# Performance work log

Measured on AMD Instinct MI355X. Metric: run time of the kernel, lower is better.

Reference implementation:

```python
import jax, jax.numpy as jnp
import numpy as np

N = 50000
E = 400000
IN_DIM = 128
HID = 128
OUT = 128
HEADS = 8
NEG_SLOPE = 0.2  # PyG GATConv default
BN_EPS = 1e-5


def _gat_conv(x, W, a_src, a_dst, b, src, dst, concat):
    """PyG GATConv (eval): self-loops added by caller. x:[N,F], W:[F,H*C], a_*:[H,C]."""
    H, C = a_src.shape
    xW = (x @ W).reshape(N, H, C)                       # [N,H,C]
    es = jnp.sum(xW * a_src[None], axis=-1)             # [N,H]
    ed = jnp.sum(xW * a_dst[None], axis=-1)             # [N,H]
    e = jax.nn.leaky_relu(es[src] + ed[dst], NEG_SLOPE) # [E,H]
    m = jax.ops.segment_max(e, dst, num_segments=N)     # softmax over incoming edges per dst
    ex = jnp.exp(e - m[dst])
    denom = jax.ops.segment_sum(ex, dst, num_segments=N)
    alpha = ex / denom[dst]                             # [E,H]
    out = jax.ops.segment_sum(xW[src] * alpha[:, :, None], dst, num_segments=N)  # [N,H,C]
    out = out.reshape(N, H * C) if concat else out.mean(axis=1)
    return out + b


def _bn_eval(h, g, be, rm, rv):
    return (h - rm) * jax.lax.rsqrt(rv + BN_EPS) * g + be


def setup_inputs() -> dict:
    key = jax.random.key(0)
    ks = jax.random.split(key, 20)
    C1 = HID // HEADS
    f32 = jnp.float32
    inp = {
        "x": jax.random.normal(ks[0], (N, IN_DIM), dtype=f32),
        "edge_index": jax.random.randint(ks[1], (2, E), 0, N, dtype=jnp.int64),
        # GAT layer 1 (in->hid, 8 heads, concat)
        "W1": jax.random.normal(ks[2], (IN_DIM, HEADS * C1), dtype=f32) * 0.05,
        "a_src1": jax.random.normal(ks[3], (HEADS, C1), dtype=f32) * 0.05,
        "a_dst1": jax.random.normal(ks[4], (HEADS, C1), dtype=f32) * 0.05,
        "b1": jnp.zeros((HEADS * C1,), dtype=f32),
        # GAT layer 2 (hid->hid, 8 heads, concat)
        "W2": jax.random.normal(ks[5], (HID, HEADS * C1), dtype=f32) * 0.05,
        "a_src2": jax.random.normal(ks[6], (HEADS, C1), dtype=f32) * 0.05,
        "a_dst2": jax.random.normal(ks[7], (HEADS, C1), dtype=f32) * 0.05,
        "b2": jnp.zeros((HEADS * C1,), dtype=f32),
        # GAT layer 3 (hid->out, 1 head, no concat)
        "W3": jax.random.normal(ks[8], (HID, OUT), dtype=f32) * 0.05,
        "a_src3": jax.random.normal(ks[9], (1, OUT), dtype=f32) * 0.05,
        "a_dst3": jax.random.normal(ks[10], (1, OUT), dtype=f32) * 0.05,
        "b3": jnp.zeros((OUT,), dtype=f32),
        # residual linears
        "R1w": jax.random.normal(ks[11], (IN_DIM, HID), dtype=f32) * 0.05,
        "R1b": jnp.zeros((HID,), dtype=f32),
        "R2w": jax.random.normal(ks[12], (HID, HID), dtype=f32) * 0.05,
        "R2b": jnp.zeros((HID,), dtype=f32),
        "R3w": jax.random.normal(ks[13], (HID, OUT), dtype=f32) * 0.05,
        "R3b": jnp.zeros((OUT,), dtype=f32),
        # batch norms (eval mode: running stats)
        "g1": jnp.ones((HID,), dtype=f32), "be1": jnp.zeros((HID,), dtype=f32),
        "rm1": jnp.zeros((HID,), dtype=f32), "rv1": jnp.ones((HID,), dtype=f32),
        "g2": jnp.ones((HID,), dtype=f32), "be2": jnp.zeros((HID,), dtype=f32),
        "rm2": jnp.zeros((HID,), dtype=f32), "rv2": jnp.ones((HID,), dtype=f32),
    }
    return inp


def reference(x, edge_index, W1, a_src1, a_dst1, b1, W2, a_src2, a_dst2, b2,
              W3, a_src3, a_dst3, b3, R1w, R1b, R2w, R2b, R3w, R3b,
              g1, be1, rm1, rv1, g2, be2, rm2, rv2):
    # PyG GATConv adds self-loops by default
    loops = jnp.arange(N, dtype=edge_index.dtype)
    src = jnp.concatenate([edge_index[0], loops])
    dst = jnp.concatenate([edge_index[1], loops])

    h = _gat_conv(x, W1, a_src1, a_dst1, b1, src, dst, concat=True) + (x @ R1w + R1b)
    h1 = jax.nn.relu(_bn_eval(h, g1, be1, rm1, rv1))  # dropout identity in eval

    h = _gat_conv(h1, W2, a_src2, a_dst2, b2, src, dst, concat=True) + (h1 @ R2w + R2b)
    h2 = jax.nn.relu(_bn_eval(h, g2, be2, rm2, rv2))

    out = _gat_conv(h2, W3, a_src3, a_dst3, b3, src, dst, concat=False) + (h2 @ R3w + R3b)
    return out
```

## Files before the change

kernel.cpp:

```cpp
#include <hip/hip_runtime.h>
#include <hip/hip_bf16.h>
#include <type_traits>

typedef __hip_bfloat16 bf16;
typedef __hip_bfloat162 bf162;
typedef short v8s __attribute__((ext_vector_type(8)));
typedef short v4s __attribute__((ext_vector_type(4)));
typedef float v4f __attribute__((ext_vector_type(4)));

#define CAP 64

__device__ __forceinline__ float lrelu(float x) { return x > 0.f ? x : 0.2f * x; }
__device__ __forceinline__ float b2f(bf16 v) { return __bfloat162float(v); }

__global__ void k_preW(const float* __restrict__ s0, const float* __restrict__ s1,
                       const float* __restrict__ s2, const float* __restrict__ s3,
                       const float* __restrict__ s4, const float* __restrict__ s5,
                       const float* __restrict__ as1, const float* __restrict__ ad1,
                       const float* __restrict__ as2, const float* __restrict__ ad2,
                       const float* __restrict__ as3, const float* __restrict__ ad3,
                       const float* b1, const float* R1b, const float* g1, const float* be1,
                       const float* rm1, const float* rv1,
                       const float* b2, const float* R2b, const float* g2, const float* be2,
                       const float* rm2, const float* rv2,
                       const float* b3, const float* R3b,
                       bf16* __restrict__ wt, float* __restrict__ prm,
                       int* __restrict__ cnt, int N) {
    int b = blockIdx.x;
    int t = threadIdx.x;
    if (b >= 7) {
        int n4 = N * 4;
        int base = ((b - 7) * 256 + t) * 4;
        int4 z = {0, 0, 0, 0};
#pragma unroll
        for (int k = 0; k < 4; ++k)
            if (base + k < n4) ((int4*)cnt)[base + k] = z;
        return;
    }
    if (b == 6) {
        int c = t;
        if (c < 128) {
            float s1v = g1[c] * rsqrtf(rv1[c] + 1e-5f);
            prm[c]       = b1[c] + R1b[c];
            prm[128 + c] = s1v;
            prm[256 + c] = be1[c] - rm1[c] * s1v;
            float s2v = g2[c] * rsqrtf(rv2[c] + 1e-5f);
            prm[384 + c] = b2[c] + R2b[c];
            prm[512 + c] = s2v;
            prm[640 + c] = be2[c] - rm2[c] * s2v;
            prm[768 + c] = b3[c] + R3b[c];
        }
        return;
    }
    const float* src;
    switch (b) {
        case 0: src = s0; break; case 1: src = s1; break; case 2: src = s2; break;
        case 3: src = s3; break; case 4: src = s4; break; default: src = s5; break;
    }
    bf16* dst = wt + (size_t)b * 18432;
    for (int i = t; i < 16384; i += 256) {
        int k = i >> 7, n = i & 127;
        dst[n * 128 + k] = __float2bfloat16(src[i]);
    }
    if ((b & 1) == 0) {
        int layer = b >> 1;
        if (layer < 2) {
            const float* asr = (layer == 0) ? as1 : as2;
            const float* ads = (layer == 0) ? ad1 : ad2;
            for (int i = t; i < 2048; i += 256) {
                int row = i >> 7, k = i & 127, h = row & 7;
                const float* av = (row < 8) ? asr : ads;
                float s = 0.f;
#pragma unroll
                for (int c = 0; c < 16; ++c) s += src[k * 128 + h * 16 + c] * av[h * 16 + c];
                dst[(128 + row) * 128 + k] = __float2bfloat16(s);
            }
        } else {
            for (int i = t; i < 2048; i += 256) {
                int row = i >> 7, k = i & 127;
                float s = 0.f;
                if (row == 0 || row == 8) {
                    const float* av = (row == 0) ? as3 : ad3;
                    for (int c = 0; c < 128; ++c) s += src[k * 128 + c] * av[c];
                }
                dst[(128 + row) * 128 + k] = __float2bfloat16(s);
            }
        }
    } else {
        for (int i = t; i < 2048; i += 256)
            dst[16384 + i] = __float2bfloat16(0.f);
    }
}

template <typename T>
__device__ __forceinline__ void gemm_body(const T* __restrict__ A,
                                          const bf16* __restrict__ BT0, const bf16* __restrict__ BT1,
                                          bf16* __restrict__ O0, bf16* __restrict__ O1,
                                          float* __restrict__ esed, float* __restrict__ es,
                                          float* __restrict__ ed,
                                          int mode, int nrows, int job, int ntiles) {
    const int y = (job >= ntiles) ? 1 : 0;
    const int tile = y ? job - ntiles : job;
    const bf16* BT = y ? BT1 : BT0;
    bf16* O = y ? O1 : O0;
    const int t = threadIdx.x;
    const int rowbase = tile * 128;
    const int wave = t >> 6, lane = t & 63, quad = lane >> 4, l16 = lane & 15;

    int gr[2], gc[2];
    gr[0] = rowbase + wave * 32 + l16; gc[0] = gr[0] < nrows ? gr[0] : nrows - 1;
    gr[1] = gr[0] + 16;                gc[1] = gr[1] < nrows ? gr[1] : nrows - 1;
    v8s afr[2][4];
    if constexpr (std::is_same<T, float>::value) {
#pragma unroll
        for (int rt = 0; rt < 2; ++rt) {
            const float* ar = A + (size_t)gc[rt] * 128 + quad * 8;
#pragma unroll
            for (int kit = 0; kit < 4; ++kit) {
                float4 u = *(const float4*)(ar + kit * 32);
                float4 w = *(const float4*)(ar + kit * 32 + 4);
                union { bf16 h[8]; v8s v; } tmp;
                tmp.h[0] = __float2bfloat16(u.x); tmp.h[1] = __float2bfloat16(u.y);
                tmp.h[2] = __float2bfloat16(u.z); tmp.h[3] = __float2bfloat16(u.w);
                tmp.h[4] = __float2bfloat16(w.x); tmp.h[5] = __float2bfloat16(w.y);
                tmp.h[6] = __float2bfloat16(w.z); tmp.h[7] = __float2bfloat16(w.w);
                afr[rt][kit] = tmp.v;
            }
        }
    } else {
#pragma unroll
        for (int rt = 0; rt < 2; ++rt) {
            const bf16* ar = A + (size_t)gc[rt] * 128 + quad * 8;
#pragma unroll
            for (int kit = 0; kit < 4; ++kit)
                afr[rt][kit] = *(const v8s*)(ar + kit * 32);
        }
    }

    v4f acc[2][9];
#pragma unroll
    for (int i = 0; i < 2; ++i)
#pragma unroll
        for (int j = 0; j < 9; ++j) acc[i][j] = (v4f){0.f, 0.f, 0.f, 0.f};

#pragma unroll
    for (int kit = 0; kit < 4; ++kit) {
        const bf16* brow = BT + (size_t)l16 * 128 + (kit * 4 + quad) * 8;
        v8s bfr[9];
#pragma unroll
        for (int ct = 0; ct < 9; ++ct)
            bfr[ct] = *(const v8s*)(brow + ct * 16 * 128);
#pragma unroll
        for (int rt = 0; rt < 2; ++rt)
#pragma unroll
            for (int ct = 0; ct < 9; ++ct)
                acc[rt][ct] = __builtin_amdgcn_mfma_f32_16x16x32_bf16(bfr[ct], afr[rt][kit], acc[rt][ct], 0, 0, 0);
    }

#pragma unroll
    for (int rt = 0; rt < 2; ++rt) {
        if (gr[rt] < nrows) {
            bf16* orow = O + (size_t)gr[rt] * 128 + quad * 4;
#pragma unroll
            for (int ct = 0; ct < 8; ++ct) {
                union { bf16 h[4]; v4s v; } pk;
#pragma unroll
                for (int r = 0; r < 4; ++r) pk.h[r] = __float2bfloat16(acc[rt][ct][r]);
                *(v4s*)(orow + ct * 16) = pk.v;
            }
            if (mode == 1 && y == 0) {
                *(v4f*)(esed + (size_t)gr[rt] * 16 + quad * 4) = acc[rt][8];
            } else if (mode == 2 && y == 0) {
                if (quad == 0) es[gr[rt]] = acc[rt][8][0];
                else if (quad == 2) ed[gr[rt]] = acc[rt][8][0];
            }
        }
    }
}

__global__ void k_fillgemm(const float* __restrict__ A,
                           const bf16* __restrict__ BT0, const bf16* __restrict__ BT1,
                           bf16* __restrict__ O0, bf16* __restrict__ O1,
                           float* __restrict__ esed, float* __restrict__ es, float* __restrict__ ed,
                           int nrows, int ntiles,
                           const int* __restrict__ ei, int* __restrict__ cnt,
                           int* __restrict__ csr, int E) {
    const int njobs = 2 * ntiles;
    if (blockIdx.x < njobs) {
        gemm_body<float>(A, BT0, BT1, O0, O1, esed, es, ed, 1, nrows, blockIdx.x, ntiles);
        return;
    }
    int base = (blockIdx.x - njobs) * 1024 + threadIdx.x * 4;
    if (base >= E) return;
    if (((E & 3) == 0) && base + 3 < E) {
        int4 s4 = *(const int4*)(ei + base);
        int4 d4 = *(const int4*)(ei + E + base);
        int p0 = atomicAdd(&cnt[(size_t)d4.x * 16], 1);
        int p1 = atomicAdd(&cnt[(size_t)d4.y * 16], 1);
        int p2 = atomicAdd(&cnt[(size_t)d4.z * 16], 1);
        int p3 = atomicAdd(&cnt[(size_t)d4.w * 16], 1);
        if (p0 < CAP) csr[d4.x * CAP + p0] = s4.x;
        if (p1 < CAP) csr[d4.y * CAP + p1] = s4.y;
        if (p2 < CAP) csr[d4.z * CAP + p2] = s4.z;
        if (p3 < CAP) csr[d4.w * CAP + p3] = s4.w;
    } else {
        for (int i = base; i < E && i < base + 4; ++i) {
            int d = ei[E + i];
            int pos = atomicAdd(&cnt[(size_t)d * 16], 1);
            if (pos < CAP) csr[d * CAP + pos] = ei[i];
        }
    }
}

__global__ void k_gemm(const bf16* __restrict__ A,
                       const bf16* __restrict__ BT0, const bf16* __restrict__ BT1,
                       bf16* __restrict__ O0, bf16* __restrict__ O1,
                       float* __restrict__ esed, float* __restrict__ es, float* __restrict__ ed,
                       int mode, int nrows, int ntiles) {
    gemm_body<bf16>(A, BT0, BT1, O0, O1, esed, es, ed, mode, nrows, blockIdx.x, ntiles);
}

__global__ void k_agg8(const bf16* __restrict__ xW, const float* __restrict__ esed,
                       const int* __restrict__ cnt, const int* __restrict__ csr,
                       const bf16* __restrict__ rres, const float* __restrict__ prm,
                       bf16* __restrict__ hout, int n) {
    int wave = threadIdx.x >> 6, lane = threadIdx.x & 63;
    int node = blockIdx.x * 4 + wave;
    if (node >= n) return;
    const int g = lane >> 4, l16 = lane & 15;
    const int c0 = l16 * 8;
    const int hc = l16 >> 1;
    const int he = lane & 7;
    float edw = esed[(size_t)node * 16 + 8 + he];
    float wselfh = __expf(lrelu(esed[(size_t)node * 16 + he] + edw));
    float acc[8]; float den = 0.f;
    v8s rv;
#pragma unroll
    for (int i = 0; i < 8; ++i) acc[i] = 0.f;
    {
        float ws = __shfl(wselfh, hc);
        if (g == 0) {
            rv = *(const v8s*)(rres + (size_t)node * 128 + c0);
            v8s xv = *(const v8s*)(xW + (size_t)node * 128 + c0);
            const bf16* xb = (const bf16*)&xv;
            den = ws;
#pragma unroll
            for (int i = 0; i < 8; ++i) acc[i] = ws * b2f(xb[i]);
        }
    }
    int deg = cnt[(size_t)node * 16]; if (deg > CAP) deg = CAP;
    const int* bucket = csr + (size_t)node * CAP;
    int idx = (lane < deg) ? bucket[lane] : node;
    for (int sub = 0; sub * 8 < deg; ++sub) {
        int j0 = sub * 8 + g, j1 = sub * 8 + 4 + g;
        int sv0 = __shfl(idx, j0);
        int sv1 = __shfl(idx, j1);
        v8s xv0 = *(const v8s*)(xW + (size_t)sv0 * 128 + c0);
        v8s xv1 = *(const v8s*)(xW + (size_t)sv1 * 128 + c0);
        int e = sub * 8 + (lane >> 3);
        int sidx = __shfl(idx, e);
        float esv = esed[(size_t)sidx * 16 + he];
        float w = (e < deg) ? __expf(lrelu(esv + edw)) : 0.f;
        float w0 = __shfl(w, g * 8 + hc);
        float w1 = __shfl(w, (4 + g) * 8 + hc);
        const bf16* xb0 = (const bf16*)&xv0;
        const bf16* xb1 = (const bf16*)&xv1;
        den += w0 + w1;
#pragma unroll
        for (int i = 0; i < 8; ++i) acc[i] += w0 * b2f(xb0[i]) + w1 * b2f(xb1[i]);
    }
    den += __shfl_xor(den, 16); den += __shfl_xor(den, 32);
#pragma unroll
    for (int i = 0; i < 8; ++i) {
        acc[i] += __shfl_xor(acc[i], 16);
        acc[i] += __shfl_xor(acc[i], 32);
    }
    if (g == 0) {
        float inv = 1.f / den;
        const bf16* rb = (const bf16*)&rv;
        bf16 outv[8];
#pragma unroll
        for (int i = 0; i < 8; ++i) {
            int c = c0 + i;
            float v = acc[i] * inv + prm[c] + b2f(rb[i]);
            v = fmaxf(v * prm[128 + c] + prm[256 + c], 0.f);
            outv[i] = __float2bfloat16(v);
        }
        *(v8s*)(hout + (size_t)node * 128 + c0) = *(v8s*)outv;
    }
}

__global__ void k_agg1(const bf16* __restrict__ xW, const float* __restrict__ es,
                       const float* __restrict__ ed,
                       const int* __restrict__ cnt, const int* __restrict__ csr,
                       const bf16* __restrict__ rres, const float* __restrict__ bias,
                       float* __restrict__ out, int n) {
    int wave = threadIdx.x >> 6, lane = threadIdx.x & 63;
    int node = blockIdx.x * 4 + wave;
    if (node >= n) return;
    const int g = lane >> 4, l16 = lane & 15;
    const int c0 = l16 * 8;
    float edv = ed[node];
    float wself = __expf(lrelu(es[node] + edv));
    float acc[8]; float den = 0.f;
    v8s rv;
#pragma unroll
    for (int i = 0; i < 8; ++i) acc[i] = 0.f;
    if (g == 0) {
        rv = *(const v8s*)(rres + (size_t)node * 128 + c0);
        v8s xv = *(const v8s*)(xW + (size_t)node * 128 + c0);
        const bf16* xb = (const bf16*)&xv;
        den = wself;
#pragma unroll
        for (int i = 0; i < 8; ++i) acc[i] = wself * b2f(xb[i]);
    }
    int deg = cnt[(size_t)node * 16]; if (deg > CAP) deg = CAP;
    const int* bucket = csr + (size_t)node * CAP;
    int idx = (lane < deg) ? bucket[lane] : node;
    float w = (lane < deg) ? __expf(lrelu(es[idx] + edv)) : 0.f;
    for (int j = 0; j < deg; j += 4) {
        int jl = j + g;
        int sv = __shfl(idx, jl);
        float wj = __shfl(w, jl);
        if (jl >= deg) wj = 0.f;
        v8s xv = *(const v8s*)(xW + (size_t)sv * 128 + c0);
        const bf16* xb = (const bf16*)&xv;
        den += wj;
#pragma unroll
        for (int i = 0; i < 8; ++i) acc[i] += wj * b2f(xb[i]);
    }
    den += __shfl_xor(den, 16); den += __shfl_xor(den, 32);
#pragma unroll
    for (int i = 0; i < 8; ++i) {
        acc[i] += __shfl_xor(acc[i], 16);
        acc[i] += __shfl_xor(acc[i], 32);
    }
    if (g == 0) {
        float inv = 1.f / den;
        const bf16* rb = (const bf16*)&rv;
        float ov[8];
#pragma unroll
        for (int i = 0; i < 8; ++i)
            ov[i] = acc[i] * inv + bias[c0 + i] + b2f(rb[i]);
        float4 o0, o1;
        o0.x = ov[0]; o0.y = ov[1]; o0.z = ov[2]; o0.w = ov[3];
        o1.x = ov[4]; o1.y = ov[5]; o1.z = ov[6]; o1.w = ov[7];
        *(float4*)(out + (size_t)node * 128 + c0) = o0;
        *(float4*)(out + (size_t)node * 128 + c0 + 4) = o1;
    }
}

extern "C" void kernel_launch(void* const* d_in, const int* in_sizes, int n_in,
                              void* d_out, int out_size, void* d_ws, size_t ws_size,
                              hipStream_t stream) {
    const float* x   = (const float*)d_in[0];
    const int*   ei  = (const int*)d_in[1];
    const float* W1  = (const float*)d_in[2];
    const float* as1 = (const float*)d_in[3];
    const float* ad1 = (const float*)d_in[4];
    const float* b1  = (const float*)d_in[5];
    const float* W2  = (const float*)d_in[6];
    const float* as2 = (const float*)d_in[7];
    const float* ad2 = (const float*)d_in[8];
    const float* b2  = (const float*)d_in[9];
    const float* W3  = (const float*)d_in[10];
    const float* as3 = (const float*)d_in[11];
    const float* ad3 = (const float*)d_in[12];
    const float* b3  = (const float*)d_in[13];
    const float* R1w = (const float*)d_in[14];
    const float* R1b = (const float*)d_in[15];
    const float* R2w = (const float*)d_in[16];
    const float* R2b = (const float*)d_in[17];
    const float* R3w = (const float*)d_in[18];
    const float* R3b = (const float*)d_in[19];
    const float* g1  = (const float*)d_in[20];
    const float* be1 = (const float*)d_in[21];
    const float* rm1 = (const float*)d_in[22];
    const float* rv1 = (const float*)d_in[23];
    const float* g2  = (const float*)d_in[24];
    const float* be2 = (const float*)d_in[25];
    const float* rm2 = (const float*)d_in[26];
    const float* rv2 = (const float*)d_in[27];

    const int N = in_sizes[0] / 128;
    const int E = in_sizes[1] / 2;

    char* p = (char*)d_ws;
    size_t off = 0;
    auto alloc = [&](size_t b) { void* r = p + off; off = (off + b + 255) & ~(size_t)255; return r; };
    int*   cnt  = (int*)alloc((size_t)N * 16 * 4);
    int*   csr  = (int*)alloc((size_t)N * CAP * 4);
    bf16*  WT   = (bf16*)alloc((size_t)6 * 18432 * 2);
    float* prm  = (float*)alloc(896 * 4);
    float* esed = (float*)alloc((size_t)N * 16 * 4);
    float* es   = (float*)alloc((size_t)N * 4);
    float* ed   = (float*)alloc((size_t)N * 4);
    bf16*  xW   = (bf16*)alloc((size_t)N * 128 * 2);
    bf16*  rres = (bf16*)alloc((size_t)N * 128 * 2);
    bf16*  hA   = (bf16*)alloc((size_t)N * 128 * 2);
    bf16*  hB   = (bf16*)alloc((size_t)N * 128 * 2);
    (void)ws_size; (void)n_in; (void)out_size;

    const int gx = (N + 127) / 128;
    const int nw = (N + 3) / 4;
    const int fb = (E + 1023) / 1024;
    const int zb = (N * 4 + 1023) / 1024;

    k_preW<<<7 + zb, 256, 0, stream>>>(W1, R1w, W2, R2w, W3, R3w,
                                       as1, ad1, as2, ad2, as3, ad3,
                                       b1, R1b, g1, be1, rm1, rv1,
                                       b2, R2b, g2, be2, rm2, rv2, b3, R3b,
                                       WT, prm, cnt, N);
    k_fillgemm<<<2 * gx + fb, 256, 0, stream>>>(x, WT, WT + 18432, xW, rres, esed, es, ed,
                                                N, gx, ei, cnt, csr, E);
    k_agg8<<<nw, 256, 0, stream>>>(xW, esed, cnt, csr, rres, prm, hA, N);
    k_gemm<<<2 * gx, 256, 0, stream>>>(hA, WT + 2 * 18432, WT + 3 * 18432, xW, rres, esed, es, ed, 1, N, gx);
    k_agg8<<<nw, 256, 0, stream>>>(xW, esed, cnt, csr, rres, prm + 384, hB, N);
    k_gemm<<<2 * gx, 256, 0, stream>>>(hB, WT + 4 * 18432, WT + 5 * 18432, xW, rres, esed, es, ed, 2, N, gx);
    k_agg1<<<nw, 256, 0, stream>>>(xW, es, ed, cnt, csr, rres, prm + 768, (float*)d_out, N);
}
```

Measured before the change: 359.3 us.

## Stage GEMM weight tile in XOR-swizzled LDS and interleave CSR-fill blocks

Each GEMM block now cooperatively copies the 144x128 bf16 transposed weight matrix into shared memory once, with an XOR swizzle to avoid bank conflicts. The MFMA B fragments are then read from LDS, so each wave no longer re-reads the weights from global/L2. In the fused first kernel, the CSR edge-fill blocks are spread evenly across the grid instead of all coming after the GEMM tiles, so atomics and MFMA work overlap. The cost is 36 KB of LDS per block, which limits occupancy, plus an extra block-wide barrier.

```diff
diff --git a/kernel.cpp b/kernel.cpp
--- a/kernel.cpp
+++ b/kernel.cpp
@@ -98,7 +98,8 @@
                                           bf16* __restrict__ O0, bf16* __restrict__ O1,
                                           float* __restrict__ esed, float* __restrict__ es,
                                           float* __restrict__ ed,
-                                          int mode, int nrows, int job, int ntiles) {
+                                          int mode, int nrows, int job, int ntiles,
+                                          bf16* Bsh) {
     const int y = (job >= ntiles) ? 1 : 0;
     const int tile = y ? job - ntiles : job;
     const bf16* BT = y ? BT1 : BT0;
@@ -137,19 +138,31 @@
         }
     }
 
+    for (int s = t; s < 288; s += 256) {
+        int r = s >> 1, hf = s & 1;
+        const float4* bsrc = (const float4*)(BT + r * 128 + hf * 64);
+#pragma unroll
+        for (int j = 0; j < 8; ++j) {
+            int c = hf * 8 + j, cp = c ^ (r & 7);
+            *(float4*)(&Bsh[r * 128 + cp * 8]) = bsrc[j];
+        }
+    }
+    __syncthreads();
+
     v4f acc[2][9];
 #pragma unroll
     for (int i = 0; i < 2; ++i)
 #pragma unroll
         for (int j = 0; j < 9; ++j) acc[i][j] = (v4f){0.f, 0.f, 0.f, 0.f};
-
 #pragma unroll
     for (int kit = 0; kit < 4; ++kit) {
-        const bf16* brow = BT + (size_t)l16 * 128 + (kit * 4 + quad) * 8;
         v8s bfr[9];
 #pragma unroll
-        for (int ct = 0; ct < 9; ++ct)
-            bfr[ct] = *(const v8s*)(brow + ct * 16 * 128);
+        for (int ct = 0; ct < 9; ++ct) {
+            int nn = ct * 16 + l16;
+            int cp = (kit * 4 + quad) ^ (nn & 7);
+            bfr[ct] = *(const v8s*)(&Bsh[nn * 128 + cp * 8]);
+        }
 #pragma unroll
         for (int rt = 0; rt < 2; ++rt)
 #pragma unroll
@@ -182,34 +195,38 @@
                            const bf16* __restrict__ BT0, const bf16* __restrict__ BT1,
                            bf16* __restrict__ O0, bf16* __restrict__ O1,
                            float* __restrict__ esed, float* __restrict__ es, float* __restrict__ ed,
-                           int nrows, int ntiles,
+                           int nrows, int ntiles, int fb,
                            const int* __restrict__ ei, int* __restrict__ cnt,
                            int* __restrict__ csr, int E) {
-    const int njobs = 2 * ntiles;
-    if (blockIdx.x < njobs) {
-        gemm_body<float>(A, BT0, BT1, O0, O1, esed, es, ed, 1, nrows, blockIdx.x, ntiles);
+    __shared__ bf16 Bsh[144 * 128];
+    const int nb = 2 * ntiles + fb;
+    const int b = blockIdx.x;
+    const int f0 = (int)(((long)b * fb) / nb);
+    const int f1 = (int)(((long)(b + 1) * fb) / nb);
+    if (f1 > f0) {
+        int base = f0 * 1024 + threadIdx.x * 4;
+        if (base >= E) return;
+        if (((E & 3) == 0) && base + 3 < E) {
+            int4 s4 = *(const int4*)(ei + base);
+            int4 d4 = *(const int4*)(ei + E + base);
+            int p0 = atomicAdd(&cnt[(size_t)d4.x * 16], 1);
+            int p1 = atomicAdd(&cnt[(size_t)d4.y * 16], 1);
+            int p2 = atomicAdd(&cnt[(size_t)d4.z * 16], 1);
+            int p3 = atomicAdd(&cnt[(size_t)d4.w * 16], 1);
+            if (p0 < CAP) csr[d4.x * CAP + p0] = s4.x;
+            if (p1 < CAP) csr[d4.y * CAP + p1] = s4.y;
+            if (p2 < CAP) csr[d4.z * CAP + p2] = s4.z;
+            if (p3 < CAP) csr[d4.w * CAP + p3] = s4.w;
+        } else {
+            for (int i = base; i < E && i < base + 4; ++i) {
+                int d = ei[E + i];
+                int pos = atomicAdd(&cnt[(size_t)d * 16], 1);
+                if (pos < CAP) csr[d * CAP + pos] = ei[i];
+            }
+        }
         return;
     }
-    int base = (blockIdx.x - njobs) * 1024 + threadIdx.x * 4;
-    if (base >= E) return;
-    if (((E & 3) == 0) && base + 3 < E) {
-        int4 s4 = *(const int4*)(ei + base);
-        int4 d4 = *(const int4*)(ei + E + base);
-        int p0 = atomicAdd(&cnt[(size_t)d4.x * 16], 1);
-        int p1 = atomicAdd(&cnt[(size_t)d4.y * 16], 1);
-        int p2 = atomicAdd(&cnt[(size_t)d4.z * 16], 1);
-        int p3 = atomicAdd(&cnt[(size_t)d4.w * 16], 1);
-        if (p0 < CAP) csr[d4.x * CAP + p0] = s4.x;
-        if (p1 < CAP) csr[d4.y * CAP + p1] = s4.y;
-        if (p2 < CAP) csr[d4.z * CAP + p2] = s4.z;
-        if (p3 < CAP) csr[d4.w * CAP + p3] = s4.w;
-    } else {
-        for (int i = base; i < E && i < base + 4; ++i) {
-            int d = ei[E + i];
-            int pos = atomicAdd(&cnt[(size_t)d * 16], 1);
-            if (pos < CAP) csr[d * CAP + pos] = ei[i];
-        }
-    }
+    gemm_body<float>(A, BT0, BT1, O0, O1, esed, es, ed, 1, nrows, b - f0, ntiles, Bsh);
 }
 
 __global__ void k_gemm(const bf16* __restrict__ A,
@@ -217,7 +234,8 @@
                        bf16* __restrict__ O0, bf16* __restrict__ O1,
                        float* __restrict__ esed, float* __restrict__ es, float* __restrict__ ed,
                        int mode, int nrows, int ntiles) {
-    gemm_body<bf16>(A, BT0, BT1, O0, O1, esed, es, ed, mode, nrows, blockIdx.x, ntiles);
+    __shared__ bf16 Bsh[144 * 128];
+    gemm_body<bf16>(A, BT0, BT1, O0, O1, esed, es, ed, mode, nrows, blockIdx.x, ntiles, Bsh);
 }
 
 __global__ void k_agg8(const bf16* __restrict__ xW, const float* __restrict__ esed,
@@ -412,7 +430,7 @@
                                        b2, R2b, g2, be2, rm2, rv2, b3, R3b,
                                        WT, prm, cnt, N);
     k_fillgemm<<<2 * gx + fb, 256, 0, stream>>>(x, WT, WT + 18432, xW, rres, esed, es, ed,
-                                                N, gx, ei, cnt, csr, E);
+                                                N, gx, fb, ei, cnt, csr, E);
     k_agg8<<<nw, 256, 0, stream>>>(xW, esed, cnt, csr, rres, prm, hA, N);
     k_gemm<<<2 * gx, 256, 0, stream>>>(hA, WT + 2 * 18432, WT + 3 * 18432, xW, rres, esed, es, ed, 1, N, gx);
     k_agg8<<<nw, 256, 0, stream>>>(xW, esed, cnt, csr, rres, prm + 384, hB, N);
```

Result: faster. 335.0 us (-6.8%).
